# Optimization experiments

Hardware: AMD Instinct MI355X
Metric: run time of the kernel (lower is better)

## Reference

```python
import jax, jax.numpy as jnp
import numpy as np

HID = 128
GRID = 8
PRED_LEN = 25


def _lstm_final(x, w_ih, w_hh, b_ih, b_hh):
    """PyTorch-style LSTM over time axis; returns final (h, c). x: [B, T, F]."""
    B = x.shape[0]
    H = w_hh.shape[1]
    # precompute input contribution for all timesteps: [B, T, 4H]
    gx = jnp.einsum('btf,gf->btg', x, w_ih) + b_ih + b_hh

    def step(carry, g):
        h, c = carry
        gates = g + h @ w_hh.T
        i, f, gg, o = jnp.split(gates, 4, axis=-1)  # torch gate order i,f,g,o
        i = jax.nn.sigmoid(i)
        f = jax.nn.sigmoid(f)
        gg = jnp.tanh(gg)
        o = jax.nn.sigmoid(o)
        c = f * c + i * gg
        h = o * jnp.tanh(c)
        return (h, c), None

    h0 = jnp.zeros((B, H), x.dtype)
    (h, c), _ = jax.lax.scan(step, (h0, h0), jnp.swapaxes(gx, 0, 1))
    return h, c


def _conv2d_same(x, w, b):
    y = jax.lax.conv_general_dilated(x, w, (1, 1), 'SAME',
                                     dimension_numbers=('NCHW', 'OIHW', 'NCHW'))
    return y + b[None, :, None, None]


def setup_inputs() -> dict:
    key = jax.random.key(0)
    ks = jax.random.split(key, 24)
    B, K, T, F = 8192, 8, 20, 7
    H = HID
    s = lambda fan: 1.0 / np.sqrt(fan)
    u = lambda k, shape, fan: jax.random.uniform(k, shape, jnp.float32, -s(fan), s(fan))
    inp = {
        'target': jax.random.normal(ks[0], (B, T, F), jnp.float32),
        'neigh_dyn': jax.random.normal(ks[1], (B, K, T, F), jnp.float32),
        'neigh_spatial': jax.random.normal(ks[2], (B, K, 2), jnp.float32),
        'lane': jax.random.normal(ks[3], (B, T), jnp.float32),
        # encoder LSTM
        'enc_w_ih': u(ks[4], (4 * H, F), H), 'enc_w_hh': u(ks[5], (4 * H, H), H),
        'enc_b_ih': u(ks[6], (4 * H,), H), 'enc_b_hh': u(ks[7], (4 * H,), H),
        # neighbor encoder LSTM
        'nb_w_ih': u(ks[8], (4 * H, F), H), 'nb_w_hh': u(ks[9], (4 * H, H), H),
        'nb_b_ih': u(ks[10], (4 * H,), H), 'nb_b_hh': u(ks[11], (4 * H,), H),
        # social conv stack
        'conv1_w': u(ks[12], (H // 2, H, 3, 3), H * 9), 'conv1_b': u(ks[13], (H // 2,), H * 9),
        'conv2_w': u(ks[14], (H // 4, H // 2, 3, 3), (H // 2) * 9), 'conv2_b': u(ks[15], (H // 4,), (H // 2) * 9),
        # fusion linear (H + H//4 -> H)
        'fus_w': u(ks[16], (H, H + H // 4), H + H // 4), 'fus_b': u(ks[17], (H,), H + H // 4),
        # decoder LSTM (input_dim 2)
        'dec_w_ih': u(ks[18], (4 * H, 2), H), 'dec_w_hh': u(ks[19], (4 * H, H), H),
        'dec_b_ih': u(ks[20], (4 * H,), H), 'dec_b_hh': u(ks[21], (4 * H,), H),
        # output linear (H -> 2)
        'out_w': u(ks[22], (2, H), H), 'out_b': u(ks[23], (2,), H),
    }
    return inp


def reference(target, neigh_dyn, neigh_spatial, lane,
              enc_w_ih, enc_w_hh, enc_b_ih, enc_b_hh,
              nb_w_ih, nb_w_hh, nb_b_ih, nb_b_hh,
              conv1_w, conv1_b, conv2_w, conv2_b,
              fus_w, fus_b,
              dec_w_ih, dec_w_hh, dec_b_ih, dec_b_hh,
              out_w, out_b):
    B = target.shape[0]
    K = neigh_dyn.shape[1]
    H = HID

    # encode target trajectory
    h_target, _ = _lstm_final(target, enc_w_ih, enc_w_hh, enc_b_ih, enc_b_hh)  # [B, H]

    # encode neighbors (shared weights) via flattening B*K
    neigh_flat = neigh_dyn.reshape(B * K, neigh_dyn.shape[2], neigh_dyn.shape[3])
    h_neigh, _ = _lstm_final(neigh_flat, nb_w_ih, nb_w_hh, nb_b_ih, nb_b_hh)
    h_neigh = h_neigh.reshape(B, K, H)

    # social pooling: scatter into [B, H, GRID, GRID]
    center = GRID // 2
    n = min(K, GRID * GRID - 1)
    idx = np.arange(n) + 1
    xs = idx % GRID
    ys = idx // GRID
    grid = jnp.zeros((B, H, GRID, GRID), target.dtype)
    grid = grid.at[:, :, center, center].set(h_target)
    grid = grid.at[:, :, ys, xs].set(jnp.swapaxes(h_neigh[:, :n, :], 1, 2))

    x = jax.nn.relu(_conv2d_same(grid, conv1_w, conv1_b))
    x = jax.nn.relu(_conv2d_same(x, conv2_w, conv2_b))
    pooled = jnp.max(x, axis=(2, 3))  # AdaptiveMaxPool2d(1) -> [B, H//4]

    fused = jnp.tanh(jnp.concatenate([h_target, pooled], axis=-1) @ fus_w.T + fus_b)

    dec_bias = dec_b_ih + dec_b_hh

    def dec_step(carry, _):
        h, c, inp = carry
        gates = inp @ dec_w_ih.T + h @ dec_w_hh.T + dec_bias
        i, f, gg, o = jnp.split(gates, 4, axis=-1)
        i = jax.nn.sigmoid(i)
        f = jax.nn.sigmoid(f)
        gg = jnp.tanh(gg)
        o = jax.nn.sigmoid(o)
        c = f * c + i * gg
        h = o * jnp.tanh(c)
        pred = h @ out_w.T + out_b  # [B, 2]
        return (h, c, pred), pred

    h0 = fused
    c0 = jnp.zeros_like(fused)
    inp0 = jnp.zeros((B, 2), target.dtype)
    _, preds = jax.lax.scan(dec_step, (h0, c0, inp0), None, length=PRED_LEN)
    return jnp.swapaxes(preds, 0, 1)  # [B, pred_len, 2]
```

## Files before the change

### kernel.cpp

```cpp
#include <hip/hip_runtime.h>

typedef _Float16 half8  __attribute__((ext_vector_type(8)));
typedef _Float16 half4v __attribute__((ext_vector_type(4)));
typedef float  floatx4  __attribute__((ext_vector_type(4)));

#define MFMA16(A,B,C) __builtin_amdgcn_mfma_f32_16x16x32_f16((A),(B),(C),0,0,0)

#define L2E  1.4426950408889634f
#define L2E2 2.8853900817779268f

__device__ __forceinline__ float sig_pre(float y){
  return __builtin_amdgcn_rcpf(1.0f + __builtin_amdgcn_exp2f(-y));
}
__device__ __forceinline__ float tanh_pre(float y){
  return 1.0f - 2.0f*__builtin_amdgcn_rcpf(1.0f + __builtin_amdgcn_exp2f(y));
}
__device__ __forceinline__ float tanh_raw(float c){
  return 1.0f - 2.0f*__builtin_amdgcn_rcpf(1.0f + __builtin_amdgcn_exp2f(L2E2*c));
}
__device__ __forceinline__ half8 ld8(const _Float16* p){
  half4v a = *(const half4v*)p;
  half4v b = *(const half4v*)(p+4);
  return __builtin_shufflevector(a,b,0,1,2,3,4,5,6,7);
}

static __device__ constexpr int DY[27] = {0,0,0,0,0,0,0,0, 1,1,1,1,1,1,1,1, 2,2, 3,3,3,4,4,4,5,5,5};
static __device__ constexpr int DX[27] = {0,1,2,3,4,5,6,7, 0,1,2,3,4,5,6,7, 0,1, 3,4,5,3,4,5,3,4,5};
static __device__ constexpr int PY[9]  = {0,0,0,0,0,0,0,1,4};
static __device__ constexpr int PX[9]  = {1,2,3,4,5,6,7,0,4};
static __device__ constexpr int OY[46] = {0,0,0,0,0,0,0,0, 1,1,1,1,1,1,1,1, 2,2,2,2,2,2,2,2,
                                          3,3,3,3,3,3,3, 4,4,4,4,4, 5,5,5,5,5, 6,6,6,6,6};
static __device__ constexpr int OX[46] = {0,1,2,3,4,5,6,7, 0,1,2,3,4,5,6,7, 0,1,2,3,4,5,6,7,
                                          0,1,2,3,4,5,6, 2,3,4,5,6, 2,3,4,5,6, 2,3,4,5,6};
__device__ constexpr int d1idx(int iy,int ix){
  return (iy<0||iy>7||ix<0||ix>7) ? -1 :
         (iy<=1) ? iy*8+ix :
         (iy==2 && ix<=1) ? 16+ix :
         (iy>=3 && iy<=5 && ix>=3 && ix<=5) ? 18+(iy-3)*3+(ix-3) : -1;
}

__global__ __launch_bounds__(512, 4) void lstm_all(
    const float* __restrict__ target, const float* __restrict__ neigh,
    const float* __restrict__ e_wih, const float* __restrict__ e_whh,
    const float* __restrict__ e_bih, const float* __restrict__ e_bhh,
    const float* __restrict__ n_wih, const float* __restrict__ n_whh,
    const float* __restrict__ n_bih, const float* __restrict__ n_bhh,
    _Float16* __restrict__ h_enc16, _Float16* __restrict__ h_nb16)
{
  __shared__ _Float16 h_lds[2][16][136];
  __shared__ _Float16 xf16[16][168];
  __shared__ __align__(16) _Float16 wihb[8][4][17][8];

  const int tid  = threadIdx.x;
  const int wv   = tid >> 6;
  const int lane = tid & 63;
  const int q    = lane >> 4;
  const int cb   = lane & 15;

  const bool enc = (blockIdx.x < 512);
  const float* x   = enc ? target : neigh;
  const float* wih = enc ? e_wih : n_wih;
  const float* whh = enc ? e_whh : n_whh;
  const float* bih = enc ? e_bih : n_bih;
  const float* bhh = enc ? e_bhh : n_bhh;
  _Float16* hout   = enc ? h_enc16 : h_nb16;
  const long base  = enc ? (long)blockIdx.x*16 : (long)(blockIdx.x-512)*16;

  for (int i = tid; i < 16*168; i += 512){
    int seq = i/168, rem = i%168, t = rem>>3, f = rem&7;
    float v = 0.f;
    if (t < 20) v = (f < 7) ? x[base*140 + seq*140 + t*7 + f] : 1.0f;
    xf16[seq][rem] = (_Float16)v;
  }
  for (int i = tid; i < 2*16*136; i += 512) ((_Float16*)h_lds)[i] = (_Float16)0.f;

  if (q == 0){
    #pragma unroll
    for (int g=0; g<4; ++g){
      const float sc = (g==2) ? L2E2 : L2E;
      const int col = g*128 + wv*16 + cb;
      _Float16* d = &wihb[wv][g][cb][0];
      #pragma unroll
      for (int j=0;j<7;++j) d[j] = (_Float16)(wih[col*7+j]*sc);
      d[7] = (_Float16)((bih[col]+bhh[col])*sc);
    }
  } else if (lane == 16){
    #pragma unroll
    for (int g=0; g<4; ++g){
      _Float16* d = &wihb[wv][g][16][0];
      #pragma unroll
      for (int j=0;j<8;++j) d[j] = (_Float16)0.f;
    }
  }

  half8 bfrag[4][4];
  #pragma unroll
  for (int g=0; g<4; ++g){
    const float sc = (g==2) ? L2E2 : L2E;
    const int col = g*128 + wv*16 + cb;
    #pragma unroll
    for (int kc=0; kc<4; ++kc){
      const float* src = whh + (long)col*128 + kc*32 + q*8;
      half8 f;
      #pragma unroll
      for (int j=0;j<8;++j) f[j] = (_Float16)(src[j]*sc);
      bfrag[g][kc] = f;
    }
  }
  __syncthreads();

  const int hcol = wv*16 + cb;
  const _Float16* bxp = &wihb[wv][0][(q==0)?cb:16][0];
  const _Float16* a4p = (q==0) ? &xf16[cb][0] : &wihb[wv][0][16][0];
  const int a4step = (q==0) ? 8 : 0;
  half8 a4 = *(const half8*)a4p;
  a4p += a4step;

  float c_reg[4] = {0,0,0,0};
  float h_new[4] = {0,0,0,0};
  const floatx4 ZERO4 = {0.f,0.f,0.f,0.f};

  for (int t=0; t<20; ++t){
    const _Float16* hrow = &h_lds[t&1][cb][0];
    _Float16 (*hw)[136]  = h_lds[(t+1)&1];

    floatx4 acc[4];
    #pragma unroll
    for (int g=0; g<4; ++g){
      half8 bx = *(const half8*)(bxp + g*136);
      acc[g] = MFMA16(a4, bx, ZERO4);
    }
    #pragma unroll
    for (int kc=0; kc<4; ++kc){
      half8 a = *(const half8*)(hrow + kc*32 + q*8);
      #pragma unroll
      for (int g=0; g<4; ++g)
        acc[g] = MFMA16(a, bfrag[g][kc], acc[g]);
    }
    #pragma unroll
    for (int r=0; r<4; ++r){
      float ig = sig_pre(acc[0][r]);
      float fg = sig_pre(acc[1][r]);
      float gg = tanh_pre(acc[2][r]);
      float og = sig_pre(acc[3][r]);
      float c  = fg*c_reg[r] + ig*gg;
      c_reg[r] = c;
      h_new[r] = og*tanh_raw(c);
    }
    #pragma unroll
    for (int r=0; r<4; ++r) hw[q*4 + r][hcol] = (_Float16)h_new[r];
    a4 = *(const half8*)a4p;
    a4p += a4step;
    __syncthreads();
  }

  #pragma unroll
  for (int r=0; r<4; ++r)
    hout[(base + q*4 + r)*128 + hcol] = (_Float16)h_new[r];
}

__global__ void prep_kernel(const float* __restrict__ w1, const float* __restrict__ b1,
                            const float* __restrict__ w2, const float* __restrict__ b2,
                            const float* __restrict__ fus_w,
                            _Float16* __restrict__ w1f, _Float16* __restrict__ w2f,
                            _Float16* __restrict__ fus_wf,
                            float* __restrict__ v2bg, float* __restrict__ bgmax)
{
  const int tid = threadIdx.x;
  const int gid = blockIdx.x*256 + tid;
  const int gstride = gridDim.x*256;
  for (int i = gid; i < 9*64*128; i += gstride){
    int s = i>>13, rem = i&8191, c1 = rem>>7, ci = rem&127;
    w1f[s*8448 + c1*132 + ci] = (_Float16)w1[c1*1152 + ci*9 + s];
  }
  for (int i = gid; i < 9*32*64; i += gstride){
    int s = i>>11, rem = i&2047, c2 = rem>>6, ci = rem&63;
    w2f[s*2176 + c2*68 + ci] = (_Float16)w2[c2*576 + ci*9 + s];
  }
  for (int i = gid; i < 128*160; i += gstride){
    int n = i/160, k = i%160;
    fus_wf[n*164 + k] = (_Float16)fus_w[i];
  }
  if (blockIdx.x == 0){
    __shared__ float S[288];
    __shared__ int bgm[32];
    for (int i=tid;i<288;i+=256){
      int c2=i/9, s=i%9;
      float a=0.f;
      for (int ci=0;ci<64;++ci) a += w2[c2*576+ci*9+s]*fmaxf(b1[ci],0.f);
      S[i]=a;
    }
    if (tid<32) bgm[tid]=0;
    __syncthreads();
    for (int i=tid;i<2048;i+=256){
      int cell=i>>5, c2=i&31, y=cell>>3, xx=cell&7;
      float a=b2[c2];
      for (int dy=0;dy<3;++dy){ int iy=y+dy-1; if((unsigned)iy>7u) continue;
        for (int dx=0;dx<3;++dx){ int ix=xx+dx-1; if((unsigned)ix>7u) continue;
          a += S[c2*9+dy*3+dx]; } }
      v2bg[cell*32+c2]=a;
      bool aff = (y<=2) || (y==3 && xx<=6) || (y>=4 && y<=6 && xx>=2 && xx<=6);
      if(!aff) atomicMax(&bgm[c2], __float_as_int(fmaxf(a,0.f)));
    }
    __syncthreads();
    if (tid<32) bgmax[tid]=__int_as_float(bgm[tid]);
  }
}

__global__ __launch_bounds__(256, 1) void social_fuse(
    const _Float16* __restrict__ h_enc, const _Float16* __restrict__ h_nb,
    const _Float16* __restrict__ w1f, const _Float16* __restrict__ w2f,
    const _Float16* __restrict__ fus_wf,
    const float* __restrict__ b1, const float* __restrict__ v2bg,
    const float* __restrict__ bgmax, const float* __restrict__ fus_b,
    float* __restrict__ fused)
{
  __shared__ __align__(16) _Float16 vecs[9*16*132];
  __shared__ __align__(16) _Float16 d1[27*16*68];
  __shared__ __align__(16) _Float16 A16[16*164];
  __shared__ int pooled[512];

  const int tid  = threadIdx.x;
  const int wv   = tid >> 6;
  const int lane = tid & 63;
  const int q    = lane >> 4;
  const int cb   = lane & 15;
  const long base = (long)blockIdx.x * 16;

  for (int i=tid; i<9*16*32; i+=256){
    int p = i>>9, rem = i&511, bb = rem>>5, j = rem&31;
    const _Float16* src = (p<8) ? (h_nb + (((base+bb))*8 + p)*128 + j*4)
                                : (h_enc + (base+bb)*128 + j*4);
    *(unsigned long long*)(vecs + p*2112 + bb*132 + j*4) = *(const unsigned long long*)src;
  }
  for (int i=tid; i<512; i+=256){
    int bb=i>>5, j=i&31;
    *(unsigned long long*)(A16 + bb*164 + j*4) =
        *(const unsigned long long*)(h_enc + (base+bb)*128 + j*4);
  }
  for (int i=tid; i<512; i+=256) pooled[i] = __float_as_int(bgmax[i&31]);
  __syncthreads();

  {
    const int c1lane = wv*16 + cb;
    half8 bf1[9][4];
    #pragma unroll
    for (int s=0;s<9;++s)
      #pragma unroll
      for (int kc=0;kc<4;++kc)
        bf1[s][kc] = ld8(w1f + s*8448 + c1lane*132 + kc*32 + q*8);
    const float b1v = b1[c1lane];
    const float bg  = fmaxf(b1v, 0.f);

    #pragma unroll
    for (int ci=0; ci<27; ++ci){
      const int y = DY[ci], x = DX[ci];
      floatx4 C = {0.f,0.f,0.f,0.f};
      #pragma unroll
      for (int p=0;p<9;++p){
        const int dy = PY[p]-y+1, dx = PX[p]-x+1;
        if (dy>=0 && dy<3 && dx>=0 && dx<3){
          const int s = dy*3+dx;
          const _Float16* ap = vecs + p*2112 + cb*132 + q*8;
          #pragma unroll
          for (int kc=0;kc<4;++kc)
            C = MFMA16(ld8(ap + kc*32), bf1[s][kc], C);
        }
      }
      _Float16* dp = d1 + ci*1088 + c1lane;
      #pragma unroll
      for (int r=0;r<4;++r)
        dp[(q*4+r)*68] = (_Float16)(fmaxf(b1v + C[r], 0.f) - bg);
    }
  }
  __syncthreads();

  {
    half8 bf2[9][2][2];
    #pragma unroll
    for (int s=0;s<9;++s)
      #pragma unroll
      for (int nt=0;nt<2;++nt)
        #pragma unroll
        for (int kc=0;kc<2;++kc)
          bf2[s][nt][kc] = ld8(w2f + s*2176 + (nt*16+cb)*68 + kc*32 + q*8);

    float rm0[4] = {0,0,0,0}, rm1[4] = {0,0,0,0};
    #pragma unroll
    for (int oc=0; oc<46; ++oc){
      if ((oc & 3) != wv) continue;
      const int y = OY[oc], x = OX[oc];
      const int cell = y*8+x;
      float v0 = v2bg[cell*32 + cb];
      float v1 = v2bg[cell*32 + 16 + cb];
      floatx4 C0 = {v0,v0,v0,v0}, C1 = {v1,v1,v1,v1};
      #pragma unroll
      for (int dy=0;dy<3;++dy)
        #pragma unroll
        for (int dx=0;dx<3;++dx){
          const int dc = d1idx(y+dy-1, x+dx-1);
          if (dc < 0) continue;
          const int s = dy*3+dx;
          const _Float16* ap = d1 + dc*1088 + cb*68 + q*8;
          #pragma unroll
          for (int kc=0;kc<2;++kc){
            half8 a = ld8(ap + kc*32);
            C0 = MFMA16(a, bf2[s][0][kc], C0);
            C1 = MFMA16(a, bf2[s][1][kc], C1);
          }
        }
      #pragma unroll
      for (int r=0;r<4;++r){
        rm0[r] = fmaxf(rm0[r], fmaxf(C0[r],0.f));
        rm1[r] = fmaxf(rm1[r], fmaxf(C1[r],0.f));
      }
    }
    #pragma unroll
    for (int r=0;r<4;++r){
      atomicMax(&pooled[(q*4+r)*32 + cb],      __float_as_int(rm0[r]));
      atomicMax(&pooled[(q*4+r)*32 + 16 + cb], __float_as_int(rm1[r]));
    }
  }
  __syncthreads();

  for (int i=tid;i<512;i+=256){
    int bb=i>>5, c2=i&31;
    A16[bb*164 + 128 + c2] = (_Float16)__int_as_float(pooled[i]);
  }
  __syncthreads();

  {
    half8 bfF[2][5];
    #pragma unroll
    for (int nt2=0;nt2<2;++nt2)
      #pragma unroll
      for (int kc=0;kc<5;++kc)
        bfF[nt2][kc] = ld8(fus_wf + ((wv*2+nt2)*16+cb)*164 + kc*32 + q*8);
    const float fb0 = fus_b[(wv*2)*16+cb];
    const float fb1 = fus_b[(wv*2+1)*16+cb];
    floatx4 C0 = {0.f,0.f,0.f,0.f}, C1 = {0.f,0.f,0.f,0.f};
    #pragma unroll
    for (int kc=0;kc<5;++kc){
      half8 a = ld8(A16 + cb*164 + kc*32 + q*8);
      C0 = MFMA16(a, bfF[0][kc], C0);
      C1 = MFMA16(a, bfF[1][kc], C1);
    }
    #pragma unroll
    for (int r=0;r<4;++r){
      const long row = base + q*4 + r;
      fused[row*128 + (wv*2)*16+cb]   = tanh_raw(C0[r]+fb0);
      fused[row*128 + (wv*2+1)*16+cb] = tanh_raw(C1[r]+fb1);
    }
  }
}

__global__ __launch_bounds__(512, 4) void dec_mfma(
    const float* __restrict__ fused,
    const float* __restrict__ w_ih, const float* __restrict__ w_hh,
    const float* __restrict__ b_ih, const float* __restrict__ b_hh,
    const float* __restrict__ out_w, const float* __restrict__ out_b,
    float* __restrict__ out)
{
  __shared__ _Float16 h_lds[2][16][136];
  __shared__ float ow_lds[2][128];
  __shared__ float pred_lds[16][2];

  const int tid  = threadIdx.x;
  const int wv   = tid >> 6;
  const int lane = tid & 63;
  const int q    = lane >> 4;
  const int cb   = lane & 15;
  const long base = (long)blockIdx.x * 16;

  for (int i=tid;i<256;i+=512) ow_lds[i>>7][i&127] = out_w[i];
  for (int i=tid;i<2048;i+=512) h_lds[0][i>>7][i&127] = (_Float16)fused[base*128 + i];
  if (tid<32) pred_lds[tid>>1][tid&1] = 0.f;

  half8 bfrag[4][4];
  float bias_g[4], wi0[4], wi1[4];
  #pragma unroll
  for (int g=0; g<4; ++g){
    const float sc = (g==2) ? L2E2 : L2E;
    const int col = g*128 + wv*16 + cb;
    bias_g[g] = (b_ih[col] + b_hh[col])*sc;
    wi0[g] = w_ih[col*2+0]*sc;
    wi1[g] = w_ih[col*2+1]*sc;
    #pragma unroll
    for (int kc=0; kc<4; ++kc){
      const float* src = w_hh + (long)col*128 + kc*32 + q*8;
      half8 f;
      #pragma unroll
      for (int j=0;j<8;++j) f[j] = (_Float16)(src[j]*sc);
      bfrag[g][kc] = f;
    }
  }
  float ob0 = out_b[0], ob1 = out_b[1];
  __syncthreads();

  const int hcol = wv*16 + cb;
  float c_reg[4] = {0,0,0,0};
  float h_new[4];

  for (int t=0; t<25; ++t){
    const _Float16 (*hr)[136] = h_lds[t&1];
    _Float16 (*hw)[136]       = h_lds[(t+1)&1];

    floatx4 acc[4];
    #pragma unroll
    for (int r=0; r<4; ++r){
      float p0 = pred_lds[q*4+r][0], p1 = pred_lds[q*4+r][1];
      #pragma unroll
      for (int g=0; g<4; ++g)
        acc[g][r] = bias_g[g] + wi0[g]*p0 + wi1[g]*p1;
    }
    #pragma unroll
    for (int kc=0; kc<4; ++kc){
      half8 a = *(const half8*)&hr[cb][kc*32 + q*8];
      #pragma unroll
      for (int g=0; g<4; ++g)
        acc[g] = MFMA16(a, bfrag[g][kc], acc[g]);
    }
    #pragma unroll
    for (int r=0; r<4; ++r){
      float ig = sig_pre(acc[0][r]);
      float fg = sig_pre(acc[1][r]);
      float gg = tanh_pre(acc[2][r]);
      float og = sig_pre(acc[3][r]);
      float c  = fg*c_reg[r] + ig*gg;
      c_reg[r] = c;
      h_new[r] = og*tanh_raw(c);
    }
    #pragma unroll
    for (int r=0; r<4; ++r) hw[q*4+r][hcol] = (_Float16)h_new[r];
    __syncthreads();
    {
      int pair = tid>>3, part = tid&7;
      if (pair < 32){
        int m = pair>>1, oc = pair&1;
        const float* owp = ow_lds[oc];
        float v = 0.f;
        #pragma unroll
        for (int k=part*16; k<part*16+16; ++k) v += owp[k]*(float)hw[m][k];
        v += __shfl_down(v, 4, 8);
        v += __shfl_down(v, 2, 8);
        v += __shfl_down(v, 1, 8);
        if (part==0){
          v += (oc ? ob1 : ob0);
          pred_lds[m][oc] = v;
          out[(base+m)*50 + t*2 + oc] = v;
        }
      }
    }
    __syncthreads();
  }
}

extern "C" void kernel_launch(void* const* d_in, const int* in_sizes, int n_in,
                              void* d_out, int out_size, void* d_ws, size_t ws_size,
                              hipStream_t stream)
{
  (void)in_sizes; (void)n_in; (void)out_size; (void)ws_size;
  const float* target   = (const float*)d_in[0];
  const float* neigh    = (const float*)d_in[1];
  const float* enc_w_ih = (const float*)d_in[4];
  const float* enc_w_hh = (const float*)d_in[5];
  const float* enc_b_ih = (const float*)d_in[6];
  const float* enc_b_hh = (const float*)d_in[7];
  const float* nb_w_ih  = (const float*)d_in[8];
  const float* nb_w_hh  = (const float*)d_in[9];
  const float* nb_b_ih  = (const float*)d_in[10];
  const float* nb_b_hh  = (const float*)d_in[11];
  const float* w1       = (const float*)d_in[12];
  const float* b1       = (const float*)d_in[13];
  const float* w2       = (const float*)d_in[14];
  const float* b2       = (const float*)d_in[15];
  const float* fus_w    = (const float*)d_in[16];
  const float* fus_b    = (const float*)d_in[17];
  const float* dec_w_ih = (const float*)d_in[18];
  const float* dec_w_hh = (const float*)d_in[19];
  const float* dec_b_ih = (const float*)d_in[20];
  const float* dec_b_hh = (const float*)d_in[21];
  const float* out_w    = (const float*)d_in[22];
  const float* out_b    = (const float*)d_in[23];

  char* ws = (char*)d_ws;
  _Float16* h_nb16  = (_Float16*)ws;
  _Float16* h_enc16 = (_Float16*)(ws + (16u<<20));
  float*    fusedp  = (float*)(ws + (18u<<20));
  char* aux = ws + (22u<<20);
  _Float16* w1f    = (_Float16*)aux;
  _Float16* w2f    = (_Float16*)(aux + 152064);
  _Float16* fus_wf = (_Float16*)(aux + 152064 + 39168);
  float*    v2bg   = (float*)(aux + 233216);
  float*    bgmaxp = (float*)(aux + 241408);

  prep_kernel<<<64, 256, 0, stream>>>(w1, b1, w2, b2, fus_w, w1f, w2f, fus_wf, v2bg, bgmaxp);
  lstm_all<<<4608, 512, 0, stream>>>(target, neigh,
                                     enc_w_ih, enc_w_hh, enc_b_ih, enc_b_hh,
                                     nb_w_ih, nb_w_hh, nb_b_ih, nb_b_hh,
                                     h_enc16, h_nb16);
  social_fuse<<<512, 256, 0, stream>>>(h_enc16, h_nb16, w1f, w2f, fus_wf,
                                       b1, v2bg, bgmaxp, fus_b, fusedp);
  dec_mfma<<<512, 512, 0, stream>>>(fusedp, dec_w_ih, dec_w_hh, dec_b_ih, dec_b_hh,
                                    out_w, out_b, (float*)d_out);
}
```

Before: 554.3 us.

## Fuse LSTM gate math with shared reciprocals and transpose MFMA operands

```diff
diff --git a/kernel.cpp b/kernel.cpp
--- a/kernel.cpp
+++ b/kernel.cpp
@@ -9,19 +9,27 @@
 #define L2E  1.4426950408889634f
 #define L2E2 2.8853900817779268f
 
-__device__ __forceinline__ float sig_pre(float y){
-  return __builtin_amdgcn_rcpf(1.0f + __builtin_amdgcn_exp2f(-y));
-}
-__device__ __forceinline__ float tanh_pre(float y){
-  return 1.0f - 2.0f*__builtin_amdgcn_rcpf(1.0f + __builtin_amdgcn_exp2f(y));
-}
+__device__ __forceinline__ float rcpf(float x){ return __builtin_amdgcn_rcpf(x); }
+__device__ __forceinline__ float ex2(float x){ return __builtin_amdgcn_exp2f(x); }
 __device__ __forceinline__ float tanh_raw(float c){
-  return 1.0f - 2.0f*__builtin_amdgcn_rcpf(1.0f + __builtin_amdgcn_exp2f(L2E2*c));
+  return 1.0f - 2.0f*rcpf(1.0f + ex2(L2E2*c));
 }
 __device__ __forceinline__ half8 ld8(const _Float16* p){
   half4v a = *(const half4v*)p;
   half4v b = *(const half4v*)(p+4);
   return __builtin_shufflevector(a,b,0,1,2,3,4,5,6,7);
+}
+
+__device__ __forceinline__ float lstm_cell(float yi, float yf, float yg, float yo,
+                                           float& c){
+  float A = ex2(-yi), B = ex2(-yf), C = ex2(yg);
+  float r1 = rcpf(1.0f + B);
+  float r2 = rcpf((1.0f + A)*(1.0f + C));
+  float cn = c*r1 + (C - 1.0f)*r2;
+  c = cn;
+  float F = ex2(-yo), E = ex2(L2E2*cn);
+  float r3 = rcpf((1.0f + F)*(1.0f + E));
+  return (E - 1.0f)*r3;
 }
 
 static __device__ constexpr int DY[27] = {0,0,0,0,0,0,0,0, 1,1,1,1,1,1,1,1, 2,2, 3,3,3,4,4,4,5,5,5};
@@ -109,7 +117,6 @@
   }
   __syncthreads();
 
-  const int hcol = wv*16 + cb;
   const _Float16* bxp = &wihb[wv][0][(q==0)?cb:16][0];
   const _Float16* a4p = (q==0) ? &xf16[cb][0] : &wihb[wv][0][16][0];
   const int a4step = (q==0) ? 8 : 0;
@@ -117,46 +124,35 @@
   a4p += a4step;
 
   float c_reg[4] = {0,0,0,0};
-  float h_new[4] = {0,0,0,0};
+  half4v hv = {0,0,0,0};
   const floatx4 ZERO4 = {0.f,0.f,0.f,0.f};
 
   for (int t=0; t<20; ++t){
     const _Float16* hrow = &h_lds[t&1][cb][0];
-    _Float16 (*hw)[136]  = h_lds[(t+1)&1];
 
     floatx4 acc[4];
     #pragma unroll
     for (int g=0; g<4; ++g){
       half8 bx = *(const half8*)(bxp + g*136);
-      acc[g] = MFMA16(a4, bx, ZERO4);
+      acc[g] = MFMA16(bx, a4, ZERO4);
     }
     #pragma unroll
     for (int kc=0; kc<4; ++kc){
-      half8 a = *(const half8*)(hrow + kc*32 + q*8);
+      half8 b = *(const half8*)(hrow + kc*32 + q*8);
       #pragma unroll
       for (int g=0; g<4; ++g)
-        acc[g] = MFMA16(a, bfrag[g][kc], acc[g]);
-    }
-    #pragma unroll
-    for (int r=0; r<4; ++r){
-      float ig = sig_pre(acc[0][r]);
-      float fg = sig_pre(acc[1][r]);
-      float gg = tanh_pre(acc[2][r]);
-      float og = sig_pre(acc[3][r]);
-      float c  = fg*c_reg[r] + ig*gg;
-      c_reg[r] = c;
-      h_new[r] = og*tanh_raw(c);
-    }
-    #pragma unroll
-    for (int r=0; r<4; ++r) hw[q*4 + r][hcol] = (_Float16)h_new[r];
+        acc[g] = MFMA16(bfrag[g][kc], b, acc[g]);
+    }
+    #pragma unroll
+    for (int r=0; r<4; ++r)
+      hv[r] = (_Float16)lstm_cell(acc[0][r], acc[1][r], acc[2][r], acc[3][r], c_reg[r]);
+    *(half4v*)&h_lds[(t+1)&1][cb][wv*16 + q*4] = hv;
     a4 = *(const half8*)a4p;
     a4p += a4step;
     __syncthreads();
   }
 
-  #pragma unroll
-  for (int r=0; r<4; ++r)
-    hout[(base + q*4 + r)*128 + hcol] = (_Float16)h_new[r];
+  *(half4v*)&hout[(base + cb)*128 + wv*16 + q*4] = hv;
 }
 
 __global__ void prep_kernel(const float* __restrict__ w1, const float* __restrict__ b1,
@@ -362,6 +358,7 @@
     float* __restrict__ out)
 {
   __shared__ _Float16 h_lds[2][16][136];
+  __shared__ __align__(16) _Float16 wib[8][4][17][8];
   __shared__ float ow_lds[2][128];
   __shared__ float pred_lds[16][2];
 
@@ -374,17 +371,35 @@
 
   for (int i=tid;i<256;i+=512) ow_lds[i>>7][i&127] = out_w[i];
   for (int i=tid;i<2048;i+=512) h_lds[0][i>>7][i&127] = (_Float16)fused[base*128 + i];
+  for (int i=tid;i<2048;i+=512) h_lds[1][i>>7][i&127] = (_Float16)0.f;
   if (tid<32) pred_lds[tid>>1][tid&1] = 0.f;
 
+  if (q == 0){
+    #pragma unroll
+    for (int g=0; g<4; ++g){
+      const float sc = (g==2) ? L2E2 : L2E;
+      const int col = g*128 + wv*16 + cb;
+      _Float16* d = &wib[wv][g][cb][0];
+      d[0] = (_Float16)(w_ih[col*2+0]*sc);
+      d[1] = (_Float16)(w_ih[col*2+1]*sc);
+      d[2] = (_Float16)((b_ih[col]+b_hh[col])*sc);
+      #pragma unroll
+      for (int j=3;j<8;++j) d[j] = (_Float16)0.f;
+    }
+  } else if (lane == 16){
+    #pragma unroll
+    for (int g=0; g<4; ++g){
+      _Float16* d = &wib[wv][g][16][0];
+      #pragma unroll
+      for (int j=0;j<8;++j) d[j] = (_Float16)0.f;
+    }
+  }
+
   half8 bfrag[4][4];
-  float bias_g[4], wi0[4], wi1[4];
   #pragma unroll
   for (int g=0; g<4; ++g){
     const float sc = (g==2) ? L2E2 : L2E;
     const int col = g*128 + wv*16 + cb;
-    bias_g[g] = (b_ih[col] + b_hh[col])*sc;
-    wi0[g] = w_ih[col*2+0]*sc;
-    wi1[g] = w_ih[col*2+1]*sc;
     #pragma unroll
     for (int kc=0; kc<4; ++kc){
       const float* src = w_hh + (long)col*128 + kc*32 + q*8;
@@ -397,41 +412,38 @@
   float ob0 = out_b[0], ob1 = out_b[1];
   __syncthreads();
 
-  const int hcol = wv*16 + cb;
+  const _Float16* wibp = &wib[wv][0][(q==0)?cb:16][0];
   float c_reg[4] = {0,0,0,0};
-  float h_new[4];
+  half4v hv;
+  const floatx4 ZERO4 = {0.f,0.f,0.f,0.f};
 
   for (int t=0; t<25; ++t){
-    const _Float16 (*hr)[136] = h_lds[t&1];
-    _Float16 (*hw)[136]       = h_lds[(t+1)&1];
-
+    const _Float16* hrow = &h_lds[t&1][cb][0];
+
+    half8 pb = {0,0,0,0,0,0,0,0};
+    if (q == 0){
+      pb[0] = (_Float16)pred_lds[cb][0];
+      pb[1] = (_Float16)pred_lds[cb][1];
+      pb[2] = (_Float16)1.0f;
+    }
     floatx4 acc[4];
     #pragma unroll
-    for (int r=0; r<4; ++r){
-      float p0 = pred_lds[q*4+r][0], p1 = pred_lds[q*4+r][1];
+    for (int g=0; g<4; ++g){
+      half8 w = *(const half8*)(wibp + g*136);
+      acc[g] = MFMA16(w, pb, ZERO4);
+    }
+    #pragma unroll
+    for (int kc=0; kc<4; ++kc){
+      half8 b = *(const half8*)(hrow + kc*32 + q*8);
       #pragma unroll
       for (int g=0; g<4; ++g)
-        acc[g][r] = bias_g[g] + wi0[g]*p0 + wi1[g]*p1;
-    }
-    #pragma unroll
-    for (int kc=0; kc<4; ++kc){
-      half8 a = *(const half8*)&hr[cb][kc*32 + q*8];
-      #pragma unroll
-      for (int g=0; g<4; ++g)
-        acc[g] = MFMA16(a, bfrag[g][kc], acc[g]);
-    }
-    #pragma unroll
-    for (int r=0; r<4; ++r){
-      float ig = sig_pre(acc[0][r]);
-      float fg = sig_pre(acc[1][r]);
-      float gg = tanh_pre(acc[2][r]);
-      float og = sig_pre(acc[3][r]);
-      float c  = fg*c_reg[r] + ig*gg;
-      c_reg[r] = c;
-      h_new[r] = og*tanh_raw(c);
-    }
-    #pragma unroll
-    for (int r=0; r<4; ++r) hw[q*4+r][hcol] = (_Float16)h_new[r];
+        acc[g] = MFMA16(bfrag[g][kc], b, acc[g]);
+    }
+    #pragma unroll
+    for (int r=0; r<4; ++r)
+      hv[r] = (_Float16)lstm_cell(acc[0][r], acc[1][r], acc[2][r], acc[3][r], c_reg[r]);
+    _Float16 (*hw)[136] = h_lds[(t+1)&1];
+    *(half4v*)&hw[cb][wv*16 + q*4] = hv;
     __syncthreads();
     {
       int pair = tid>>3, part = tid&7;
```

Result: faster. 526.9 us (-4.9%).
